# Kernel tuning notes

Hardware: AMD Instinct MI355X
Metric: run time of the kernel (lower is better)

## Reference

```python
import jax, jax.numpy as jnp
import numpy as np

HIDDEN = 128
E = 400000
NUM_GRAPHS = 512


def setup_inputs() -> dict:
    key = jax.random.key(0)
    ks = jax.random.split(key, 9)
    src = jax.random.normal(ks[0], (E, HIDDEN), dtype=jnp.float32)
    dst = jax.random.normal(ks[1], (E, HIDDEN), dtype=jnp.float32)
    edge_attr = jax.random.normal(ks[2], (E, HIDDEN), dtype=jnp.float32)
    u = jax.random.normal(ks[3], (NUM_GRAPHS, HIDDEN), dtype=jnp.float32)
    batch = jnp.sort(jax.random.randint(ks[4], (E,), 0, NUM_GRAPHS, dtype=jnp.int64))
    # MLP params: Linear(4*hidden -> hidden), ReLU, Linear(hidden -> hidden)
    in_dim = 4 * HIDDEN
    lim1 = 1.0 / np.sqrt(in_dim)
    lim2 = 1.0 / np.sqrt(HIDDEN)
    W1 = jax.random.uniform(ks[5], (in_dim, HIDDEN), minval=-lim1, maxval=lim1, dtype=jnp.float32)
    b1 = jax.random.uniform(ks[6], (HIDDEN,), minval=-lim1, maxval=lim1, dtype=jnp.float32)
    W2 = jax.random.uniform(ks[7], (HIDDEN, HIDDEN), minval=-lim2, maxval=lim2, dtype=jnp.float32)
    b2 = jax.random.uniform(ks[8], (HIDDEN,), minval=-lim2, maxval=lim2, dtype=jnp.float32)
    return {"src": src, "dst": dst, "edge_attr": edge_attr, "u": u,
            "batch": batch, "W1": W1, "b1": b1, "W2": W2, "b2": b2}


def reference(src, dst, edge_attr, u, batch, W1, b1, W2, b2):
    # gather global feature per edge, concat, 2-layer MLP
    x = jnp.concatenate([src, dst, edge_attr, u[batch]], axis=-1)  # [E, 4*hidden]
    h = jax.nn.relu(x @ W1 + b1)  # [E, hidden]
    return h @ W2 + b2            # [E, hidden]
```

## Files before the change

kernel.cpp:

```cpp
#include <hip/hip_runtime.h>
#include <hip/hip_bf16.h>

#define HID 128

typedef __attribute__((ext_vector_type(4)))  float f32x4;
typedef __attribute__((ext_vector_type(16))) float f32x16;
typedef __attribute__((ext_vector_type(8)))  short short8;

static __device__ __forceinline__ unsigned short f2bf_u(float f) {
  unsigned u = __builtin_bit_cast(unsigned, f);
  return (unsigned short)((u + 0x7fffu + ((u >> 16) & 1u)) >> 16);
}

static __device__ __forceinline__ unsigned pk2(float a, float b) {
  return (unsigned)f2bf_u(a) | ((unsigned)f2bf_u(b) << 16);
}

static __device__ __forceinline__ short f2bf(float f) {
  return (short)f2bf_u(f);
}

static __device__ __forceinline__ short8 pack8(const f32x4 x, const f32x4 y) {
  union { unsigned u[4]; short8 s; } r;
  r.u[0] = pk2(x[0], x[1]); r.u[1] = pk2(x[2], x[3]);
  r.u[2] = pk2(y[0], y[1]); r.u[3] = pk2(y[2], y[3]);
  return r.s;
}

__global__ void prep_uc(const float* __restrict__ u, const float* __restrict__ W1,
                        const float* __restrict__ b1, float* __restrict__ Uc) {
  __shared__ float us[HID];
  const int g = blockIdx.x, n = threadIdx.x;
  us[n] = u[g * HID + n];
  __syncthreads();
  float acc = b1[n];
  const float* w = W1 + 3 * HID * HID + n;
  #pragma unroll 8
  for (int k = 0; k < HID; ++k) acc += us[k] * w[k * HID];
  Uc[g * HID + n] = acc;
}

__global__ __launch_bounds__(256, 2) void edge_mlp(
    const float* __restrict__ src, const float* __restrict__ dst,
    const float* __restrict__ ea, const int* __restrict__ batch,
    const float* __restrict__ W1, const float* __restrict__ W2,
    const float* __restrict__ b2, const float* __restrict__ Uc,
    float* __restrict__ out, int E, int nTiles) {
  __shared__ __align__(16) short hlds[64 * HID];

  const int lane = threadIdx.x & 63;
  const int wave = threadIdx.x >> 6;
  const int l31  = lane & 31;
  const int kh   = lane >> 5;
  const int ncol = wave * 32 + l31;

  short8 B1f[24];
  #pragma unroll
  for (int s = 0; s < 24; ++s) {
    const float* p = W1 + (long)(s * 16 + kh * 8) * HID + ncol;
    union { unsigned u[4]; short8 s8; } r;
    #pragma unroll
    for (int j = 0; j < 4; ++j)
      r.u[j] = pk2(p[(long)(2 * j) * HID], p[(long)(2 * j + 1) * HID]);
    B1f[s] = r.s8;
  }
  short8 B2f[8];
  #pragma unroll
  for (int s = 0; s < 8; ++s) {
    const float* p = W2 + (long)(s * 16 + kh * 8) * HID + ncol;
    union { unsigned u[4]; short8 s8; } r;
    #pragma unroll
    for (int j = 0; j < 4; ++j)
      r.u[j] = pk2(p[(long)(2 * j) * HID], p[(long)(2 * j + 1) * HID]);
    B2f[s] = r.s8;
  }
  const float b2v = b2[ncol];

  for (int t = blockIdx.x; t < nTiles; t += gridDim.x) {
    const int e0 = t * 64;
    const int rA = min(e0 + l31,      E - 1);
    const int rB = min(e0 + 32 + l31, E - 1);

    f32x16 acc0, acc1;
    #pragma unroll
    for (int i = 0; i < 16; ++i) { acc0[i] = 0.f; acc1[i] = 0.f; }

    const float* const SRC3[3] = {src, dst, ea};
    #pragma unroll
    for (int c = 0; c < 3; ++c) {
      const float* pa = SRC3[c] + (long)rA * HID + kh * 8;
      const float* pb = SRC3[c] + (long)rB * HID + kh * 8;
      #pragma unroll
      for (int ss = 0; ss < 8; ++ss) {
        const f32x4 xa0 = *(const f32x4*)(pa + ss * 16);
        const f32x4 xa1 = *(const f32x4*)(pa + ss * 16 + 4);
        const f32x4 xb0 = *(const f32x4*)(pb + ss * 16);
        const f32x4 xb1 = *(const f32x4*)(pb + ss * 16 + 4);
        const short8 a0 = pack8(xa0, xa1);
        const short8 a1 = pack8(xb0, xb1);
        acc0 = __builtin_amdgcn_mfma_f32_32x32x16_bf16(a0, B1f[c * 8 + ss], acc0, 0, 0, 0);
        acc1 = __builtin_amdgcn_mfma_f32_32x32x16_bf16(a1, B1f[c * 8 + ss], acc1, 0, 0, 0);
      }
    }

    const int gA = batch[min(e0, E - 1)];
    const int gB = batch[min(e0 + 63, E - 1)];
    if (gA == gB) {
      const float ucv = Uc[(long)gA * HID + ncol];
      #pragma unroll
      for (int i = 0; i < 16; ++i) { acc0[i] += ucv; acc1[i] += ucv; }
    } else {
      #pragma unroll
      for (int i = 0; i < 16; ++i) {
        const int crow = (i & 3) + 8 * (i >> 2) + 4 * kh;
        acc0[i] += Uc[(long)batch[min(e0 + crow,      E - 1)] * HID + ncol];
        acc1[i] += Uc[(long)batch[min(e0 + 32 + crow, E - 1)] * HID + ncol];
      }
    }

    #pragma unroll
    for (int i = 0; i < 16; ++i) {
      const int crow = (i & 3) + 8 * (i >> 2) + 4 * kh;
      const int R0 = crow, R1 = 32 + crow;
      hlds[R0 * HID + (ncol ^ ((R0 & 7) << 3))] = f2bf(fmaxf(acc0[i], 0.f));
      hlds[R1 * HID + (ncol ^ ((R1 & 7) << 3))] = f2bf(fmaxf(acc1[i], 0.f));
    }
    __syncthreads();

    f32x16 o0, o1;
    #pragma unroll
    for (int i = 0; i < 16; ++i) { o0[i] = 0.f; o1[i] = 0.f; }
    #pragma unroll
    for (int s = 0; s < 8; ++s) {
      const int k0 = s * 16 + kh * 8;
      const int RA2 = l31, RB2 = 32 + l31;
      const short8 ha = *(const short8*)&hlds[RA2 * HID + (k0 ^ ((RA2 & 7) << 3))];
      const short8 hb = *(const short8*)&hlds[RB2 * HID + (k0 ^ ((RB2 & 7) << 3))];
      o0 = __builtin_amdgcn_mfma_f32_32x32x16_bf16(ha, B2f[s], o0, 0, 0, 0);
      o1 = __builtin_amdgcn_mfma_f32_32x32x16_bf16(hb, B2f[s], o1, 0, 0, 0);
    }

    #pragma unroll
    for (int i = 0; i < 16; ++i) {
      const int crow = (i & 3) + 8 * (i >> 2) + 4 * kh;
      const int eA = e0 + crow, eB = e0 + 32 + crow;
      if (eA < E) out[(long)eA * HID + ncol] = o0[i] + b2v;
      if (eB < E) out[(long)eB * HID + ncol] = o1[i] + b2v;
    }
    __syncthreads();
  }
}

extern "C" void kernel_launch(void* const* d_in, const int* in_sizes, int n_in,
                              void* d_out, int out_size, void* d_ws, size_t ws_size,
                              hipStream_t stream) {
  const float* src   = (const float*)d_in[0];
  const float* dst   = (const float*)d_in[1];
  const float* ea    = (const float*)d_in[2];
  const float* u     = (const float*)d_in[3];
  const int*   batch = (const int*)d_in[4];
  const float* W1    = (const float*)d_in[5];
  const float* b1    = (const float*)d_in[6];
  const float* W2    = (const float*)d_in[7];
  const float* b2    = (const float*)d_in[8];
  float* out = (float*)d_out;
  float* Uc  = (float*)d_ws;

  const int E = in_sizes[0] / HID;
  const int G = in_sizes[3] / HID;

  prep_uc<<<G, HID, 0, stream>>>(u, W1, b1, Uc);

  const int nTiles = (E + 63) / 64;
  const int grid = nTiles < 1024 ? nTiles : 1024;
  edge_mlp<<<grid, 256, 0, stream>>>(src, dst, ea, batch, W1, W2, b2, Uc, out, E, nTiles);
}
```

Baseline: 735.3 us.

## Stage edge tiles through double-buffered LDS with prefetch and hardware bf16 packing

Inputs are now loaded cooperatively with coalesced vector loads into registers for the next tile. They are converted with the v_cvt_pk_bf16_f32 instruction and written into a swizzled, double-buffered LDS buffer while the current tile is computed. Tiles shrink from 64 to 32 edges and the grid shrinks from 1024 to 512 blocks. The goal is to overlap global memory latency with MFMA work and to replace the software bf16 rounding. The costs are extra LDS traffic and register pressure from the staging registers, plus less per-wave MFMA work per tile.

```diff
diff --git a/kernel.cpp b/kernel.cpp
--- a/kernel.cpp
+++ b/kernel.cpp
@@ -1,30 +1,16 @@
 #include <hip/hip_runtime.h>
-#include <hip/hip_bf16.h>
 
 #define HID 128
 
 typedef __attribute__((ext_vector_type(4)))  float f32x4;
 typedef __attribute__((ext_vector_type(16))) float f32x16;
 typedef __attribute__((ext_vector_type(8)))  short short8;
-
-static __device__ __forceinline__ unsigned short f2bf_u(float f) {
-  unsigned u = __builtin_bit_cast(unsigned, f);
-  return (unsigned short)((u + 0x7fffu + ((u >> 16) & 1u)) >> 16);
-}
-
-static __device__ __forceinline__ unsigned pk2(float a, float b) {
-  return (unsigned)f2bf_u(a) | ((unsigned)f2bf_u(b) << 16);
-}
-
-static __device__ __forceinline__ short f2bf(float f) {
-  return (short)f2bf_u(f);
-}
-
-static __device__ __forceinline__ short8 pack8(const f32x4 x, const f32x4 y) {
-  union { unsigned u[4]; short8 s; } r;
-  r.u[0] = pk2(x[0], x[1]); r.u[1] = pk2(x[2], x[3]);
-  r.u[2] = pk2(y[0], y[1]); r.u[3] = pk2(y[2], y[3]);
-  return r.s;
+typedef __attribute__((ext_vector_type(4)))  short short4v;
+
+static __device__ __forceinline__ unsigned cvt_pk_bf16(float lo, float hi) {
+  unsigned r;
+  asm("v_cvt_pk_bf16_f32 %0, %1, %2" : "=v"(r) : "v"(lo), "v"(hi));
+  return r;
 }
 
 __global__ void prep_uc(const float* __restrict__ u, const float* __restrict__ W1,
@@ -46,109 +32,146 @@
     const float* __restrict__ W1, const float* __restrict__ W2,
     const float* __restrict__ b2, const float* __restrict__ Uc,
     float* __restrict__ out, int E, int nTiles) {
-  __shared__ __align__(16) short hlds[64 * HID];
-
-  const int lane = threadIdx.x & 63;
-  const int wave = threadIdx.x >> 6;
+  __shared__ __align__(16) short Abuf[2][48 * 32 * 8];
+  __shared__ __align__(16) short hbuf[16 * 32 * 8];
+
+  const int tid  = threadIdx.x;
+  const int lane = tid & 63;
+  const int wave = tid >> 6;
   const int l31  = lane & 31;
   const int kh   = lane >> 5;
   const int ncol = wave * 32 + l31;
+  const int cst  = (tid & 31) * 4;
+  const int rb   = tid >> 5;
+
+  if (blockIdx.x >= nTiles) return;
+
+  f32x4 stg[12];
+  #define STAGE_ISSUE(e0)                                                      \
+    _Pragma("unroll")                                                          \
+    for (int i = 0; i < 12; ++i) {                                             \
+      const int a  = (i * 256 + tid) >> 10;                                    \
+      const int r  = (i * 8 + rb) & 31;                                        \
+      const int rg = min((e0) + r, E - 1);                                     \
+      const float* gp = (a == 0 ? src : (a == 1 ? dst : ea));                  \
+      stg[i] = *(const f32x4*)(gp + (long)rg * HID + cst);                     \
+    }
+
+  #define STAGE_WRITE(pb)                                                      \
+    _Pragma("unroll")                                                          \
+    for (int i = 0; i < 12; ++i) {                                             \
+      const int a   = (i * 256 + tid) >> 10;                                   \
+      const int r   = (i * 8 + rb) & 31;                                       \
+      const int c16 = a * 16 + (cst >> 3);                                     \
+      const int off = c16 * 256 + ((r ^ (c16 & 7)) << 3) + (cst & 4);          \
+      union { unsigned u[2]; short4v s; } wpk;                                 \
+      wpk.u[0] = cvt_pk_bf16(stg[i][0], stg[i][1]);                           \
+      wpk.u[1] = cvt_pk_bf16(stg[i][2], stg[i][3]);                           \
+      *(short4v*)&Abuf[pb][off] = wpk.s;                                       \
+    }
+
+  int t = blockIdx.x;
+  const int G = gridDim.x;
+  int p = 0;
+
+  STAGE_ISSUE(t * 32)
 
   short8 B1f[24];
   #pragma unroll
   for (int s = 0; s < 24; ++s) {
-    const float* p = W1 + (long)(s * 16 + kh * 8) * HID + ncol;
+    const float* pw = W1 + (long)(s * 16 + kh * 8) * HID + ncol;
     union { unsigned u[4]; short8 s8; } r;
     #pragma unroll
     for (int j = 0; j < 4; ++j)
-      r.u[j] = pk2(p[(long)(2 * j) * HID], p[(long)(2 * j + 1) * HID]);
+      r.u[j] = cvt_pk_bf16(pw[(long)(2 * j) * HID], pw[(long)(2 * j + 1) * HID]);
     B1f[s] = r.s8;
   }
   short8 B2f[8];
   #pragma unroll
   for (int s = 0; s < 8; ++s) {
-    const float* p = W2 + (long)(s * 16 + kh * 8) * HID + ncol;
+    const float* pw = W2 + (long)(s * 16 + kh * 8) * HID + ncol;
     union { unsigned u[4]; short8 s8; } r;
     #pragma unroll
     for (int j = 0; j < 4; ++j)
-      r.u[j] = pk2(p[(long)(2 * j) * HID], p[(long)(2 * j + 1) * HID]);
+      r.u[j] = cvt_pk_bf16(pw[(long)(2 * j) * HID], pw[(long)(2 * j + 1) * HID]);
     B2f[s] = r.s8;
   }
   const float b2v = b2[ncol];
 
-  for (int t = blockIdx.x; t < nTiles; t += gridDim.x) {
-    const int e0 = t * 64;
-    const int rA = min(e0 + l31,      E - 1);
-    const int rB = min(e0 + 32 + l31, E - 1);
-
-    f32x16 acc0, acc1;
-    #pragma unroll
-    for (int i = 0; i < 16; ++i) { acc0[i] = 0.f; acc1[i] = 0.f; }
-
-    const float* const SRC3[3] = {src, dst, ea};
-    #pragma unroll
-    for (int c = 0; c < 3; ++c) {
-      const float* pa = SRC3[c] + (long)rA * HID + kh * 8;
-      const float* pb = SRC3[c] + (long)rB * HID + kh * 8;
-      #pragma unroll
-      for (int ss = 0; ss < 8; ++ss) {
-        const f32x4 xa0 = *(const f32x4*)(pa + ss * 16);
-        const f32x4 xa1 = *(const f32x4*)(pa + ss * 16 + 4);
-        const f32x4 xb0 = *(const f32x4*)(pb + ss * 16);
-        const f32x4 xb1 = *(const f32x4*)(pb + ss * 16 + 4);
-        const short8 a0 = pack8(xa0, xa1);
-        const short8 a1 = pack8(xb0, xb1);
-        acc0 = __builtin_amdgcn_mfma_f32_32x32x16_bf16(a0, B1f[c * 8 + ss], acc0, 0, 0, 0);
-        acc1 = __builtin_amdgcn_mfma_f32_32x32x16_bf16(a1, B1f[c * 8 + ss], acc1, 0, 0, 0);
-      }
-    }
-
-    const int gA = batch[min(e0, E - 1)];
-    const int gB = batch[min(e0 + 63, E - 1)];
+  STAGE_WRITE(0)
+  asm volatile("s_waitcnt lgkmcnt(0)" ::: "memory");
+  __builtin_amdgcn_s_barrier();
+
+  while (true) {
+    const int e0 = t * 32;
+    const int tn = t + G;
+    const bool more = (tn < nTiles);
+    if (more) STAGE_ISSUE(tn * 32)
+
+    f32x16 acc;
+    #pragma unroll
+    for (int i = 0; i < 16; ++i) acc[i] = 0.f;
+    #pragma unroll
+    for (int s = 0; s < 24; ++s) {
+      const int c16 = 2 * s + kh;
+      const short8 af = *(const short8*)&Abuf[p][c16 * 256 + ((l31 ^ (c16 & 7)) << 3)];
+      acc = __builtin_amdgcn_mfma_f32_32x32x16_bf16(af, B1f[s], acc, 0, 0, 0);
+    }
+
+    const int gA = batch[e0];
+    const int gB = batch[min(e0 + 31, E - 1)];
     if (gA == gB) {
       const float ucv = Uc[(long)gA * HID + ncol];
       #pragma unroll
-      for (int i = 0; i < 16; ++i) { acc0[i] += ucv; acc1[i] += ucv; }
+      for (int i = 0; i < 16; ++i) acc[i] += ucv;
     } else {
       #pragma unroll
       for (int i = 0; i < 16; ++i) {
         const int crow = (i & 3) + 8 * (i >> 2) + 4 * kh;
-        acc0[i] += Uc[(long)batch[min(e0 + crow,      E - 1)] * HID + ncol];
-        acc1[i] += Uc[(long)batch[min(e0 + 32 + crow, E - 1)] * HID + ncol];
+        acc[i] += Uc[(long)batch[min(e0 + crow, E - 1)] * HID + ncol];
       }
+    }
+
+    const int hc = ncol >> 3;
+    const int hs = ncol & 7;
+    #pragma unroll
+    for (int j = 0; j < 8; ++j) {
+      const int i0 = 2 * j;
+      const int r0 = (i0 & 3) + 8 * (i0 >> 2) + 4 * kh;
+      const unsigned pk = cvt_pk_bf16(fmaxf(acc[i0], 0.f), fmaxf(acc[i0 + 1], 0.f));
+      hbuf[hc * 256 + ((r0 ^ (hc & 7)) << 3) + hs]       = (short)(pk & 0xffffu);
+      hbuf[hc * 256 + (((r0 + 1) ^ (hc & 7)) << 3) + hs] = (short)(pk >> 16);
+    }
+
+    asm volatile("s_waitcnt lgkmcnt(0)" ::: "memory");
+    __builtin_amdgcn_s_barrier();
+
+    f32x16 o;
+    #pragma unroll
+    for (int i = 0; i < 16; ++i) o[i] = 0.f;
+    #pragma unroll
+    for (int s = 0; s < 8; ++s) {
+      const int c16 = 2 * s + kh;
+      const short8 hf = *(const short8*)&hbuf[c16 * 256 + ((l31 ^ (c16 & 7)) << 3)];
+      o = __builtin_amdgcn_mfma_f32_32x32x16_bf16(hf, B2f[s], o, 0, 0, 0);
     }
 
     #pragma unroll
     for (int i = 0; i < 16; ++i) {
       const int crow = (i & 3) + 8 * (i >> 2) + 4 * kh;
-      const int R0 = crow, R1 = 32 + crow;
-      hlds[R0 * HID + (ncol ^ ((R0 & 7) << 3))] = f2bf(fmaxf(acc0[i], 0.f));
-      hlds[R1 * HID + (ncol ^ ((R1 & 7) << 3))] = f2bf(fmaxf(acc1[i], 0.f));
-    }
-    __syncthreads();
-
-    f32x16 o0, o1;
-    #pragma unroll
-    for (int i = 0; i < 16; ++i) { o0[i] = 0.f; o1[i] = 0.f; }
-    #pragma unroll
-    for (int s = 0; s < 8; ++s) {
-      const int k0 = s * 16 + kh * 8;
-      const int RA2 = l31, RB2 = 32 + l31;
-      const short8 ha = *(const short8*)&hlds[RA2 * HID + (k0 ^ ((RA2 & 7) << 3))];
-      const short8 hb = *(const short8*)&hlds[RB2 * HID + (k0 ^ ((RB2 & 7) << 3))];
-      o0 = __builtin_amdgcn_mfma_f32_32x32x16_bf16(ha, B2f[s], o0, 0, 0, 0);
-      o1 = __builtin_amdgcn_mfma_f32_32x32x16_bf16(hb, B2f[s], o1, 0, 0, 0);
-    }
-
-    #pragma unroll
-    for (int i = 0; i < 16; ++i) {
-      const int crow = (i & 3) + 8 * (i >> 2) + 4 * kh;
-      const int eA = e0 + crow, eB = e0 + 32 + crow;
-      if (eA < E) out[(long)eA * HID + ncol] = o0[i] + b2v;
-      if (eB < E) out[(long)eB * HID + ncol] = o1[i] + b2v;
-    }
-    __syncthreads();
+      const int e = e0 + crow;
+      if (e < E) out[(long)e * HID + ncol] = o[i] + b2v;
+    }
+
+    if (!more) break;
+    STAGE_WRITE(p ^ 1)
+    asm volatile("s_waitcnt lgkmcnt(0)" ::: "memory");
+    __builtin_amdgcn_s_barrier();
+    p ^= 1;
+    t = tn;
   }
+  #undef STAGE_ISSUE
+  #undef STAGE_WRITE
 }
 
 extern "C" void kernel_launch(void* const* d_in, const int* in_sizes, int n_in,
@@ -171,7 +194,7 @@
 
   prep_uc<<<G, HID, 0, stream>>>(u, W1, b1, Uc);
 
-  const int nTiles = (E + 63) / 64;
-  const int grid = nTiles < 1024 ? nTiles : 1024;
+  const int nTiles = (E + 31) / 32;
+  const int grid = nTiles < 512 ? nTiles : 512;
   edge_mlp<<<grid, 256, 0, stream>>>(src, dst, ea, batch, W1, W2, b2, Uc, out, E, nTiles);
 }
```

New measurement: 621.2 us. 1.18x faster.
